# Kernel tuning notes

Measured on AMD Instinct MI355X. Metric: run time of the kernel, lower is better.

Reference implementation:

```python
import jax, jax.numpy as jnp
import numpy as np

N = 50000   # nodes
E = 600000  # edges
F = 128     # num_node_features
H = 128     # hidden_channels
C = 10      # num_classes
G = 64      # graphs in batch


def setup_inputs() -> dict:
    key = jax.random.key(0)
    ks = jax.random.split(key, 12)
    x = jax.random.normal(ks[0], (N, F), jnp.float32)
    edge_index = jax.random.randint(ks[1], (2, E), 0, N, dtype=jnp.int32)
    batch = jnp.sort(jax.random.randint(ks[2], (N,), 0, G, dtype=jnp.int32))
    def glorot(k, shape):
        lim = np.sqrt(6.0 / (shape[0] + shape[1])).astype(np.float32)
        return jax.random.uniform(k, shape, jnp.float32, -lim, lim)
    return {
        "x": x,
        "edge_index": edge_index,
        "batch": batch,
        "W1": glorot(ks[3], (F, H)), "b1": jnp.zeros((H,), jnp.float32),
        "W2": glorot(ks[4], (H, H)), "b2": jnp.zeros((H,), jnp.float32),
        "W3": glorot(ks[5], (H, H)), "b3": jnp.zeros((H,), jnp.float32),
        "Wl": glorot(ks[6], (H, C)), "bl": jnp.zeros((C,), jnp.float32),
    }


def reference(x, edge_index, batch, W1, b1, W2, b2, W3, b3, Wl, bl):
    # GCNConv: add self-loops, symmetric degree normalization D^-1/2 A D^-1/2
    src0, dst0 = edge_index[0], edge_index[1]
    loop = jnp.arange(N, dtype=src0.dtype)
    src = jnp.concatenate([src0, loop])
    dst = jnp.concatenate([dst0, loop])
    deg = jax.ops.segment_sum(jnp.ones_like(dst, jnp.float32), dst, num_segments=N)
    dinv = jnp.where(deg > 0, jax.lax.rsqrt(deg), 0.0)
    norm = dinv[src] * dinv[dst]  # [E+N]

    def conv(h, W, b):
        h = h @ W                                  # [N, H] transform first (PyG GCNConv)
        msg = h[src] * norm[:, None]               # gather + normalize
        return jax.ops.segment_sum(msg, dst, num_segments=N) + b  # scatter-add

    h = jax.nn.relu(conv(x, W1, b1))
    h = jax.nn.relu(conv(h, W2, b2))
    h = conv(h, W3, b3)

    # global_mean_pool over batch ids
    counts = jax.ops.segment_sum(jnp.ones((N,), jnp.float32), batch, num_segments=G)
    pooled = jax.ops.segment_sum(h, batch, num_segments=G) / jnp.maximum(counts, 1.0)[:, None]
    return pooled @ Wl + bl  # [G, C]
```

## Files before the change

kernel.cpp:

```cpp
#include <hip/hip_runtime.h>
#include <hip/hip_bf16.h>

#define NN 50000
#define EE 600000
#define FF 128
#define HH 128
#define CC 10
#define GG 64

typedef unsigned int uint32;
typedef unsigned short ushort16;
typedef __attribute__((ext_vector_type(8))) short short8;
typedef __attribute__((ext_vector_type(4))) float f32x4;

__device__ __forceinline__ float bf_lo(uint32 u) { return __uint_as_float(u << 16); }
__device__ __forceinline__ float bf_hi(uint32 u) { return __uint_as_float(u & 0xffff0000u); }
__device__ __forceinline__ ushort16 f2bf(float f) {
    __hip_bfloat16 b = __float2bfloat16(f);
    return *reinterpret_cast<ushort16*>(&b);
}
__device__ __forceinline__ uint32 pack2bf(float a, float b) {
    return (uint32)f2bf(a) | ((uint32)f2bf(b) << 16);
}

__global__ void count_deg(const int* __restrict__ dst, int* __restrict__ deg) {
    int e = blockIdx.x * blockDim.x + threadIdx.x;
    if (e < EE) atomicAdd(&deg[dst[e]], 1);
}

__global__ void compute_dinv(const int* __restrict__ deg, float* __restrict__ dinv) {
    int n = blockIdx.x * blockDim.x + threadIdx.x;
    if (n < NN) dinv[n] = rsqrtf((float)(deg[n] + 1));
}

#define SB 256
__global__ __launch_bounds__(SB) void scan_block(const int* __restrict__ deg,
                                                 int* __restrict__ row_ptr,
                                                 int* __restrict__ bsum) {
    __shared__ int sm[SB];
    int t = threadIdx.x;
    int i = blockIdx.x * SB + t;
    int v = (i < NN) ? deg[i] : 0;
    sm[t] = v;
    __syncthreads();
    for (int off = 1; off < SB; off <<= 1) {
        int add = (t >= off) ? sm[t - off] : 0;
        __syncthreads();
        sm[t] += add;
        __syncthreads();
    }
    if (i < NN) row_ptr[i] = sm[t] - v;
    if (t == SB - 1) bsum[blockIdx.x] = sm[t];
}

__global__ void scan_bsum(int* __restrict__ bsum, int nb) {
    __shared__ int sm[256];
    int t = threadIdx.x;
    int v = (t < nb) ? bsum[t] : 0;
    sm[t] = v;
    __syncthreads();
    for (int off = 1; off < 256; off <<= 1) {
        int add = (t >= off) ? sm[t - off] : 0;
        __syncthreads();
        sm[t] += add;
        __syncthreads();
    }
    if (t < nb) bsum[t] = sm[t] - v;
}

__global__ __launch_bounds__(SB) void scan_add(int* __restrict__ row_ptr,
                                               const int* __restrict__ bsum) {
    int i = blockIdx.x * SB + threadIdx.x;
    if (i < NN) row_ptr[i] += bsum[blockIdx.x];
    if (i == 0) row_ptr[NN] = EE;
}

__global__ void fill_csr(const int* __restrict__ src, const int* __restrict__ dst,
                         const int* __restrict__ row_ptr, int* __restrict__ cursor,
                         const float* __restrict__ dinv,
                         int2* __restrict__ csr_en) {
    int e = blockIdx.x * blockDim.x + threadIdx.x;
    if (e < EE) {
        int s = src[e], d = dst[e];
        int pos = row_ptr[d] + atomicAdd(&cursor[d], 1);
        csr_en[pos] = make_int2(s * 256, __float_as_int(dinv[s] * dinv[d]));
    }
}

__global__ __launch_bounds__(256) void cast_x(const float* __restrict__ x, uint4* __restrict__ xb) {
    int idx = blockIdx.x * 256 + threadIdx.x;
    const float4* x4 = (const float4*)x;
    float4 a = x4[2 * idx];
    float4 b = x4[2 * idx + 1];
    uint4 o;
    o.x = pack2bf(a.x, a.y);
    o.y = pack2bf(a.z, a.w);
    o.z = pack2bf(b.x, b.y);
    o.w = pack2bf(b.z, b.w);
    xb[idx] = o;
}

__global__ __launch_bounds__(256) void transpose_w(const float* __restrict__ W,
                                                   ushort16* __restrict__ Wt) {
    int base = blockIdx.x * 256 + threadIdx.x;
#pragma unroll
    for (int i = 0; i < 4; i++) {
        int idx = base + i * 4096;
        int col = idx & 127;
        int k = idx >> 7;
        Wt[col * 128 + k] = f2bf(W[k * 128 + col]);
    }
}

__global__ __launch_bounds__(256) void gemm_mfma(const ushort16* __restrict__ A,
                                                 const ushort16* __restrict__ Wt,
                                                 ushort16* __restrict__ out) {
    __shared__ uint4 lds4[34816 / 16];
    char* lds = (char*)lds4;
    int t = threadIdx.x;
    int w = t >> 6, l = t & 63;
    int lrow = l & 15, g = l >> 4;
    int rowBase = blockIdx.x * 64;
    int arow = rowBase + w * 16 + lrow;
    short8 afr[4];
    const char* Ab = (const char*)A;
    bool inb = arow < NN;
#pragma unroll
    for (int s = 0; s < 4; s++) {
        if (inb) {
            afr[s] = *(const short8*)(Ab + (size_t)arow * 256 + s * 64 + g * 16);
        } else {
            short8 z = {0, 0, 0, 0, 0, 0, 0, 0};
            afr[s] = z;
        }
    }
    const char* Wb = (const char*)Wt;
#pragma unroll
    for (int i = 0; i < 8; i++) {
        int idx = t + i * 256;
        int col = idx >> 4, c16 = idx & 15;
        *(uint4*)(lds + col * 272 + c16 * 16) = *(const uint4*)(Wb + col * 256 + c16 * 16);
    }
    __syncthreads();
    f32x4 acc[8];
#pragma unroll
    for (int c = 0; c < 8; c++) { f32x4 z = {0.f, 0.f, 0.f, 0.f}; acc[c] = z; }
#pragma unroll
    for (int s = 0; s < 4; s++) {
#pragma unroll
        for (int c = 0; c < 8; c++) {
            short8 b = *(const short8*)(lds + (c * 16 + lrow) * 272 + s * 64 + g * 16);
            acc[c] = __builtin_amdgcn_mfma_f32_16x16x32_bf16(afr[s], b, acc[c], 0, 0, 0);
        }
    }
    __syncthreads();
    char* myl = lds + w * 8448;
#pragma unroll
    for (int c = 0; c < 8; c++) {
#pragma unroll
        for (int j = 0; j < 4; j++) {
            *(float*)(myl + (g * 4 + j) * 528 + (c * 16 + lrow) * 4) = acc[c][j];
        }
    }
    __syncthreads();
#pragma unroll
    for (int j = 0; j < 8; j++) {
        int rl = (l >> 5) + 2 * j;
        int ch = l & 31;
        float4 v = *(const float4*)(myl + rl * 528 + ch * 16);
        int grow = rowBase + w * 16 + rl;
        if (grow < NN) {
            uint2 o = make_uint2(pack2bf(v.x, v.y), pack2bf(v.z, v.w));
            *(uint2*)((char*)out + (size_t)grow * 256 + ch * 8) = o;
        }
    }
}

__global__ __launch_bounds__(256) void aggregate(const ushort16* __restrict__ hW,
                                                 const int* __restrict__ row_ptr,
                                                 const int2* __restrict__ csr_en,
                                                 const float* __restrict__ dinv,
                                                 const float* __restrict__ bias,
                                                 ushort16* __restrict__ out, int relu) {
    int grp = threadIdx.x >> 4;
    int ll  = threadIdx.x & 15;
    int n = blockIdx.x * 16 + grp;
    if (n >= NN) return;
    const char* base = (const char*)hW;
    int boff = ll << 4;
    float dn = dinv[n];
    float w2 = dn * dn;
    float a0, a1, a2, a3, a4, a5, a6, a7;
    {
        uint4 u = *(const uint4*)(base + (size_t)n * 256 + boff);
        a0 = w2 * bf_lo(u.x); a1 = w2 * bf_hi(u.x);
        a2 = w2 * bf_lo(u.y); a3 = w2 * bf_hi(u.y);
        a4 = w2 * bf_lo(u.z); a5 = w2 * bf_hi(u.z);
        a6 = w2 * bf_lo(u.w); a7 = w2 * bf_hi(u.w);
    }
    int s = row_ptr[n], e = row_ptr[n + 1];
    int k = s;
    for (; k + 4 <= e; k += 4) {
        int2 c0 = csr_en[k], c1 = csr_en[k + 1], c2 = csr_en[k + 2], c3 = csr_en[k + 3];
        uint4 v0 = *(const uint4*)(base + (size_t)(uint32)c0.x + boff);
        uint4 v1 = *(const uint4*)(base + (size_t)(uint32)c1.x + boff);
        uint4 v2 = *(const uint4*)(base + (size_t)(uint32)c2.x + boff);
        uint4 v3 = *(const uint4*)(base + (size_t)(uint32)c3.x + boff);
        float n0 = __int_as_float(c0.y), n1 = __int_as_float(c1.y);
        float n2 = __int_as_float(c2.y), n3 = __int_as_float(c3.y);
        a0 += n0 * bf_lo(v0.x); a1 += n0 * bf_hi(v0.x);
        a2 += n0 * bf_lo(v0.y); a3 += n0 * bf_hi(v0.y);
        a4 += n0 * bf_lo(v0.z); a5 += n0 * bf_hi(v0.z);
        a6 += n0 * bf_lo(v0.w); a7 += n0 * bf_hi(v0.w);
        a0 += n1 * bf_lo(v1.x); a1 += n1 * bf_hi(v1.x);
        a2 += n1 * bf_lo(v1.y); a3 += n1 * bf_hi(v1.y);
        a4 += n1 * bf_lo(v1.z); a5 += n1 * bf_hi(v1.z);
        a6 += n1 * bf_lo(v1.w); a7 += n1 * bf_hi(v1.w);
        a0 += n2 * bf_lo(v2.x); a1 += n2 * bf_hi(v2.x);
        a2 += n2 * bf_lo(v2.y); a3 += n2 * bf_hi(v2.y);
        a4 += n2 * bf_lo(v2.z); a5 += n2 * bf_hi(v2.z);
        a6 += n2 * bf_lo(v2.w); a7 += n2 * bf_hi(v2.w);
        a0 += n3 * bf_lo(v3.x); a1 += n3 * bf_hi(v3.x);
        a2 += n3 * bf_lo(v3.y); a3 += n3 * bf_hi(v3.y);
        a4 += n3 * bf_lo(v3.z); a5 += n3 * bf_hi(v3.z);
        a6 += n3 * bf_lo(v3.w); a7 += n3 * bf_hi(v3.w);
    }
    for (; k < e; k++) {
        int2 c0 = csr_en[k];
        uint4 v0 = *(const uint4*)(base + (size_t)(uint32)c0.x + boff);
        float n0 = __int_as_float(c0.y);
        a0 += n0 * bf_lo(v0.x); a1 += n0 * bf_hi(v0.x);
        a2 += n0 * bf_lo(v0.y); a3 += n0 * bf_hi(v0.y);
        a4 += n0 * bf_lo(v0.z); a5 += n0 * bf_hi(v0.z);
        a6 += n0 * bf_lo(v0.w); a7 += n0 * bf_hi(v0.w);
    }
    float4 bA = *(const float4*)(bias + ll * 8);
    float4 bB = *(const float4*)(bias + ll * 8 + 4);
    a0 += bA.x; a1 += bA.y; a2 += bA.z; a3 += bA.w;
    a4 += bB.x; a5 += bB.y; a6 += bB.z; a7 += bB.w;
    if (relu) {
        a0 = fmaxf(a0, 0.f); a1 = fmaxf(a1, 0.f); a2 = fmaxf(a2, 0.f); a3 = fmaxf(a3, 0.f);
        a4 = fmaxf(a4, 0.f); a5 = fmaxf(a5, 0.f); a6 = fmaxf(a6, 0.f); a7 = fmaxf(a7, 0.f);
    }
    uint4 o;
    o.x = pack2bf(a0, a1); o.y = pack2bf(a2, a3);
    o.z = pack2bf(a4, a5); o.w = pack2bf(a6, a7);
    *(uint4*)((char*)out + (size_t)n * 256 + boff) = o;
}

#define PCH 32
__global__ __launch_bounds__(256) void pool_partial(const uint32* __restrict__ h32,
                                                    const int* __restrict__ batch,
                                                    float* __restrict__ pooled) {
    int wave = threadIdx.x >> 6;
    int lane = threadIdx.x & 63;
    int chunk = blockIdx.x * 4 + wave;
    int n0 = chunk * PCH;
    if (n0 >= NN) return;
    int n1 = n0 + PCH;
    if (n1 > NN) n1 = NN;
    int cur = batch[n0];
    float a0 = 0.f, a1 = 0.f;
    for (int n = n0; n < n1; n++) {
        int g = batch[n];
        if (g != cur) {
            atomicAdd(&pooled[cur * HH + 2 * lane], a0);
            atomicAdd(&pooled[cur * HH + 2 * lane + 1], a1);
            a0 = a1 = 0.f;
            cur = g;
        }
        uint32 v = h32[(size_t)n * 64 + lane];
        a0 += bf_lo(v);
        a1 += bf_hi(v);
    }
    atomicAdd(&pooled[cur * HH + 2 * lane], a0);
    atomicAdd(&pooled[cur * HH + 2 * lane + 1], a1);
}

__global__ __launch_bounds__(128) void final_linear(const float* __restrict__ pooled,
                                                    const int* __restrict__ batch,
                                                    const float* __restrict__ Wl,
                                                    const float* __restrict__ bl,
                                                    float* __restrict__ out) {
    int g = blockIdx.x;
    int t = threadIdx.x;
    __shared__ float pm[128];
    __shared__ int cnt_s;
    if (t == 0) {
        int lo = 0, hi = NN;
        while (lo < hi) { int m = (lo + hi) >> 1; if (batch[m] < g) lo = m + 1; else hi = m; }
        int s = lo;
        lo = 0; hi = NN;
        while (lo < hi) { int m = (lo + hi) >> 1; if (batch[m] < g + 1) lo = m + 1; else hi = m; }
        int c = lo - s;
        cnt_s = c > 0 ? c : 1;
    }
    __syncthreads();
    pm[t] = pooled[g * HH + t] / (float)cnt_s;
    __syncthreads();
    if (t < CC) {
        float o = bl[t];
        for (int f = 0; f < 128; f++) o += pm[f] * Wl[f * CC + t];
        out[g * CC + t] = o;
    }
}

extern "C" void kernel_launch(void* const* d_in, const int* in_sizes, int n_in,
                              void* d_out, int out_size, void* d_ws, size_t ws_size,
                              hipStream_t stream) {
    const float* x    = (const float*)d_in[0];
    const int*   ei   = (const int*)d_in[1];
    const int*   bat  = (const int*)d_in[2];
    const float* W1   = (const float*)d_in[3];
    const float* b1   = (const float*)d_in[4];
    const float* W2   = (const float*)d_in[5];
    const float* b2   = (const float*)d_in[6];
    const float* W3   = (const float*)d_in[7];
    const float* b3   = (const float*)d_in[8];
    const float* Wl   = (const float*)d_in[9];
    const float* bl   = (const float*)d_in[10];
    float* out = (float*)d_out;

    const int* src = ei;
    const int* dst = ei + EE;

    char* ws = (char*)d_ws;
    size_t off = 0;
    auto take = [&](size_t bytes) -> char* {
        char* p = ws + off;
        off += (bytes + 255) & ~(size_t)255;
        return p;
    };
    int*      deg     = (int*)take((size_t)NN * 4);
    float*    dinv    = (float*)take((size_t)NN * 4);
    int*      row_ptr = (int*)take((size_t)(NN + 1) * 4);
    int*      bsum    = (int*)take((size_t)256 * 4);
    int2*     csr_en  = (int2*)take((size_t)EE * 8);
    ushort16* xb      = (ushort16*)take((size_t)NN * FF * 2);
    ushort16* Wt1     = (ushort16*)take((size_t)HH * HH * 2);
    ushort16* Wt2     = (ushort16*)take((size_t)HH * HH * 2);
    ushort16* Wt3     = (ushort16*)take((size_t)HH * HH * 2);
    ushort16* bufA    = (ushort16*)take((size_t)NN * HH * 2);
    ushort16* bufB    = (ushort16*)take((size_t)NN * HH * 2);
    float*    pooled  = (float*)take((size_t)GG * HH * 4);

    const int nbScan = (NN + SB - 1) / SB;

    hipMemsetAsync(deg, 0, (size_t)NN * 4, stream);
    hipMemsetAsync(pooled, 0, (size_t)GG * HH * 4, stream);
    count_deg<<<(EE + 255) / 256, 256, 0, stream>>>(dst, deg);
    compute_dinv<<<(NN + 255) / 256, 256, 0, stream>>>(deg, dinv);
    scan_block<<<nbScan, SB, 0, stream>>>(deg, row_ptr, bsum);
    scan_bsum<<<1, 256, 0, stream>>>(bsum, nbScan);
    scan_add<<<nbScan, SB, 0, stream>>>(row_ptr, bsum);
    hipMemsetAsync(deg, 0, (size_t)NN * 4, stream);
    fill_csr<<<(EE + 255) / 256, 256, 0, stream>>>(src, dst, row_ptr, deg, dinv, csr_en);

    cast_x<<<(NN * FF / 8 + 255) / 256, 256, 0, stream>>>(x, (uint4*)xb);
    transpose_w<<<16, 256, 0, stream>>>(W1, Wt1);
    transpose_w<<<16, 256, 0, stream>>>(W2, Wt2);
    transpose_w<<<16, 256, 0, stream>>>(W3, Wt3);

    const int gemmBlocks = (NN + 63) / 64;
    const int aggBlocks  = (NN + 15) / 16;
    gemm_mfma<<<gemmBlocks, 256, 0, stream>>>(xb, Wt1, bufB);
    aggregate<<<aggBlocks, 256, 0, stream>>>(bufB, row_ptr, csr_en, dinv, b1, bufA, 1);
    gemm_mfma<<<gemmBlocks, 256, 0, stream>>>(bufA, Wt2, bufB);
    aggregate<<<aggBlocks, 256, 0, stream>>>(bufB, row_ptr, csr_en, dinv, b2, bufA, 1);
    gemm_mfma<<<gemmBlocks, 256, 0, stream>>>(bufA, Wt3, bufB);
    aggregate<<<aggBlocks, 256, 0, stream>>>(bufB, row_ptr, csr_en, dinv, b3, bufA, 0);

    const int poolBlocks = ((NN + PCH - 1) / PCH + 3) / 4;
    pool_partial<<<poolBlocks, 256, 0, stream>>>((const uint32*)bufA, bat, pooled);
    final_linear<<<GG, 128, 0, stream>>>(pooled, bat, Wl, bl, out);
}
```

Baseline: 230.1 us.

## Fuse x cast into first GEMM, pooling into last aggregate, merge transposes

Removes the separate fp32-to-bf16 cast of x by having the first GEMM load fp32 rows and convert in registers. Fuses global mean pooling into the final aggregate kernel using an LDS partial sum per block, with global atomics as the fallback, which removes the bf16 write and re-read of the last layer output. Merges the three weight transposes into one launch and software-pipelines the gather loop in aggregate. The bounds check is dropped on the assumption that NN is divisible by 16, and the final layer's pooling now sums fp32 values rather than bf16-rounded ones.

```diff
diff --git a/kernel.cpp b/kernel.cpp
--- a/kernel.cpp
+++ b/kernel.cpp
@@ -87,32 +87,27 @@
     }
 }
 
-__global__ __launch_bounds__(256) void cast_x(const float* __restrict__ x, uint4* __restrict__ xb) {
-    int idx = blockIdx.x * 256 + threadIdx.x;
-    const float4* x4 = (const float4*)x;
-    float4 a = x4[2 * idx];
-    float4 b = x4[2 * idx + 1];
-    uint4 o;
-    o.x = pack2bf(a.x, a.y);
-    o.y = pack2bf(a.z, a.w);
-    o.z = pack2bf(b.x, b.y);
-    o.w = pack2bf(b.z, b.w);
-    xb[idx] = o;
-}
-
-__global__ __launch_bounds__(256) void transpose_w(const float* __restrict__ W,
-                                                   ushort16* __restrict__ Wt) {
-    int base = blockIdx.x * 256 + threadIdx.x;
+__global__ __launch_bounds__(256) void transpose_w3(const float* __restrict__ W1,
+                                                    const float* __restrict__ W2,
+                                                    const float* __restrict__ W3,
+                                                    ushort16* __restrict__ T1,
+                                                    ushort16* __restrict__ T2,
+                                                    ushort16* __restrict__ T3) {
+    int wi = blockIdx.x >> 4;
+    const float* W = (wi == 0) ? W1 : (wi == 1) ? W2 : W3;
+    ushort16* T = (wi == 0) ? T1 : (wi == 1) ? T2 : T3;
+    int base = (blockIdx.x & 15) * 256 + threadIdx.x;
 #pragma unroll
     for (int i = 0; i < 4; i++) {
         int idx = base + i * 4096;
         int col = idx & 127;
         int k = idx >> 7;
-        Wt[col * 128 + k] = f2bf(W[k * 128 + col]);
-    }
-}
-
-__global__ __launch_bounds__(256) void gemm_mfma(const ushort16* __restrict__ A,
+        T[col * 128 + k] = f2bf(W[k * 128 + col]);
+    }
+}
+
+template <bool AF32>
+__global__ __launch_bounds__(256) void gemm_mfma(const void* __restrict__ Av,
                                                  const ushort16* __restrict__ Wt,
                                                  ushort16* __restrict__ out) {
     __shared__ uint4 lds4[34816 / 16];
@@ -123,12 +118,23 @@
     int rowBase = blockIdx.x * 64;
     int arow = rowBase + w * 16 + lrow;
     short8 afr[4];
-    const char* Ab = (const char*)A;
+    const char* Ab = (const char*)Av;
     bool inb = arow < NN;
 #pragma unroll
     for (int s = 0; s < 4; s++) {
         if (inb) {
-            afr[s] = *(const short8*)(Ab + (size_t)arow * 256 + s * 64 + g * 16);
+            if (AF32) {
+                float4 f0 = *(const float4*)(Ab + (size_t)arow * 512 + s * 128 + g * 32);
+                float4 f1 = *(const float4*)(Ab + (size_t)arow * 512 + s * 128 + g * 32 + 16);
+                union { short8 s8; uint32 u[4]; } cv;
+                cv.u[0] = pack2bf(f0.x, f0.y);
+                cv.u[1] = pack2bf(f0.z, f0.w);
+                cv.u[2] = pack2bf(f1.x, f1.y);
+                cv.u[3] = pack2bf(f1.z, f1.w);
+                afr[s] = cv.s8;
+            } else {
+                afr[s] = *(const short8*)(Ab + (size_t)arow * 256 + s * 64 + g * 16);
+            }
         } else {
             short8 z = {0, 0, 0, 0, 0, 0, 0, 0};
             afr[s] = z;
@@ -176,16 +182,27 @@
     }
 }
 
+#define AGG_FMA(c, v)                                          \
+    {                                                          \
+        float nm = __int_as_float(c.y);                        \
+        a0 += nm * bf_lo(v.x); a1 += nm * bf_hi(v.x);          \
+        a2 += nm * bf_lo(v.y); a3 += nm * bf_hi(v.y);          \
+        a4 += nm * bf_lo(v.z); a5 += nm * bf_hi(v.z);          \
+        a6 += nm * bf_lo(v.w); a7 += nm * bf_hi(v.w);          \
+    }
+
+template <int MODE>
 __global__ __launch_bounds__(256) void aggregate(const ushort16* __restrict__ hW,
                                                  const int* __restrict__ row_ptr,
                                                  const int2* __restrict__ csr_en,
                                                  const float* __restrict__ dinv,
                                                  const float* __restrict__ bias,
-                                                 ushort16* __restrict__ out, int relu) {
+                                                 ushort16* __restrict__ out,
+                                                 float* __restrict__ pooled,
+                                                 const int* __restrict__ batch) {
     int grp = threadIdx.x >> 4;
     int ll  = threadIdx.x & 15;
     int n = blockIdx.x * 16 + grp;
-    if (n >= NN) return;
     const char* base = (const char*)hW;
     int boff = ll << 4;
     float dn = dinv[n];
@@ -200,81 +217,71 @@
     }
     int s = row_ptr[n], e = row_ptr[n + 1];
     int k = s;
-    for (; k + 4 <= e; k += 4) {
+    if (k + 4 <= e) {
         int2 c0 = csr_en[k], c1 = csr_en[k + 1], c2 = csr_en[k + 2], c3 = csr_en[k + 3];
         uint4 v0 = *(const uint4*)(base + (size_t)(uint32)c0.x + boff);
         uint4 v1 = *(const uint4*)(base + (size_t)(uint32)c1.x + boff);
         uint4 v2 = *(const uint4*)(base + (size_t)(uint32)c2.x + boff);
         uint4 v3 = *(const uint4*)(base + (size_t)(uint32)c3.x + boff);
-        float n0 = __int_as_float(c0.y), n1 = __int_as_float(c1.y);
-        float n2 = __int_as_float(c2.y), n3 = __int_as_float(c3.y);
-        a0 += n0 * bf_lo(v0.x); a1 += n0 * bf_hi(v0.x);
-        a2 += n0 * bf_lo(v0.y); a3 += n0 * bf_hi(v0.y);
-        a4 += n0 * bf_lo(v0.z); a5 += n0 * bf_hi(v0.z);
-        a6 += n0 * bf_lo(v0.w); a7 += n0 * bf_hi(v0.w);
-        a0 += n1 * bf_lo(v1.x); a1 += n1 * bf_hi(v1.x);
-        a2 += n1 * bf_lo(v1.y); a3 += n1 * bf_hi(v1.y);
-        a4 += n1 * bf_lo(v1.z); a5 += n1 * bf_hi(v1.z);
-        a6 += n1 * bf_lo(v1.w); a7 += n1 * bf_hi(v1.w);
-        a0 += n2 * bf_lo(v2.x); a1 += n2 * bf_hi(v2.x);
-        a2 += n2 * bf_lo(v2.y); a3 += n2 * bf_hi(v2.y);
-        a4 += n2 * bf_lo(v2.z); a5 += n2 * bf_hi(v2.z);
-        a6 += n2 * bf_lo(v2.w); a7 += n2 * bf_hi(v2.w);
-        a0 += n3 * bf_lo(v3.x); a1 += n3 * bf_hi(v3.x);
-        a2 += n3 * bf_lo(v3.y); a3 += n3 * bf_hi(v3.y);
-        a4 += n3 * bf_lo(v3.z); a5 += n3 * bf_hi(v3.z);
-        a6 += n3 * bf_lo(v3.w); a7 += n3 * bf_hi(v3.w);
+        k += 4;
+        for (; k + 4 <= e; k += 4) {
+            int2 d0 = csr_en[k], d1 = csr_en[k + 1], d2 = csr_en[k + 2], d3 = csr_en[k + 3];
+            uint4 w0 = *(const uint4*)(base + (size_t)(uint32)d0.x + boff);
+            uint4 w1 = *(const uint4*)(base + (size_t)(uint32)d1.x + boff);
+            uint4 w2_ = *(const uint4*)(base + (size_t)(uint32)d2.x + boff);
+            uint4 w3 = *(const uint4*)(base + (size_t)(uint32)d3.x + boff);
+            AGG_FMA(c0, v0); AGG_FMA(c1, v1); AGG_FMA(c2, v2); AGG_FMA(c3, v3);
+            c0 = d0; c1 = d1; c2 = d2; c3 = d3;
+            v0 = w0; v1 = w1; v2 = w2_; v3 = w3;
+        }
+        AGG_FMA(c0, v0); AGG_FMA(c1, v1); AGG_FMA(c2, v2); AGG_FMA(c3, v3);
     }
     for (; k < e; k++) {
         int2 c0 = csr_en[k];
         uint4 v0 = *(const uint4*)(base + (size_t)(uint32)c0.x + boff);
-        float n0 = __int_as_float(c0.y);
-        a0 += n0 * bf_lo(v0.x); a1 += n0 * bf_hi(v0.x);
-        a2 += n0 * bf_lo(v0.y); a3 += n0 * bf_hi(v0.y);
-        a4 += n0 * bf_lo(v0.z); a5 += n0 * bf_hi(v0.z);
-        a6 += n0 * bf_lo(v0.w); a7 += n0 * bf_hi(v0.w);
+        AGG_FMA(c0, v0);
     }
     float4 bA = *(const float4*)(bias + ll * 8);
     float4 bB = *(const float4*)(bias + ll * 8 + 4);
     a0 += bA.x; a1 += bA.y; a2 += bA.z; a3 += bA.w;
     a4 += bB.x; a5 += bB.y; a6 += bB.z; a7 += bB.w;
-    if (relu) {
+    if (MODE == 0) {
         a0 = fmaxf(a0, 0.f); a1 = fmaxf(a1, 0.f); a2 = fmaxf(a2, 0.f); a3 = fmaxf(a3, 0.f);
         a4 = fmaxf(a4, 0.f); a5 = fmaxf(a5, 0.f); a6 = fmaxf(a6, 0.f); a7 = fmaxf(a7, 0.f);
-    }
-    uint4 o;
-    o.x = pack2bf(a0, a1); o.y = pack2bf(a2, a3);
-    o.z = pack2bf(a4, a5); o.w = pack2bf(a6, a7);
-    *(uint4*)((char*)out + (size_t)n * 256 + boff) = o;
-}
-
-#define PCH 32
-__global__ __launch_bounds__(256) void pool_partial(const uint32* __restrict__ h32,
-                                                    const int* __restrict__ batch,
-                                                    float* __restrict__ pooled) {
-    int wave = threadIdx.x >> 6;
-    int lane = threadIdx.x & 63;
-    int chunk = blockIdx.x * 4 + wave;
-    int n0 = chunk * PCH;
-    if (n0 >= NN) return;
-    int n1 = n0 + PCH;
-    if (n1 > NN) n1 = NN;
-    int cur = batch[n0];
-    float a0 = 0.f, a1 = 0.f;
-    for (int n = n0; n < n1; n++) {
+        uint4 o;
+        o.x = pack2bf(a0, a1); o.y = pack2bf(a2, a3);
+        o.z = pack2bf(a4, a5); o.w = pack2bf(a6, a7);
+        *(uint4*)((char*)out + (size_t)n * 256 + boff) = o;
+    }
+    if (MODE == 2) {
+        __shared__ float psum[4][128];
+        __shared__ int sgmin;
         int g = batch[n];
-        if (g != cur) {
-            atomicAdd(&pooled[cur * HH + 2 * lane], a0);
-            atomicAdd(&pooled[cur * HH + 2 * lane + 1], a1);
-            a0 = a1 = 0.f;
-            cur = g;
-        }
-        uint32 v = h32[(size_t)n * 64 + lane];
-        a0 += bf_lo(v);
-        a1 += bf_hi(v);
-    }
-    atomicAdd(&pooled[cur * HH + 2 * lane], a0);
-    atomicAdd(&pooled[cur * HH + 2 * lane + 1], a1);
+        if (threadIdx.x == 0) sgmin = g;
+        for (int j = threadIdx.x; j < 512; j += 256) ((float*)psum)[j] = 0.f;
+        __syncthreads();
+        int slot = g - sgmin;
+        if (slot < 4) {
+            float* p = &psum[slot][ll * 8];
+            atomicAdd(p + 0, a0); atomicAdd(p + 1, a1);
+            atomicAdd(p + 2, a2); atomicAdd(p + 3, a3);
+            atomicAdd(p + 4, a4); atomicAdd(p + 5, a5);
+            atomicAdd(p + 6, a6); atomicAdd(p + 7, a7);
+        } else {
+            float* p = &pooled[g * HH + ll * 8];
+            atomicAdd(p + 0, a0); atomicAdd(p + 1, a1);
+            atomicAdd(p + 2, a2); atomicAdd(p + 3, a3);
+            atomicAdd(p + 4, a4); atomicAdd(p + 5, a5);
+            atomicAdd(p + 6, a6); atomicAdd(p + 7, a7);
+        }
+        __syncthreads();
+        for (int j = threadIdx.x; j < 512; j += 256) {
+            int sl = j >> 7, f = j & 127;
+            float v = psum[sl][f];
+            int gg = sgmin + sl;
+            if (v != 0.f && gg < GG) atomicAdd(&pooled[gg * HH + f], v);
+        }
+    }
 }
 
 __global__ __launch_bounds__(128) void final_linear(const float* __restrict__ pooled,
@@ -336,7 +343,6 @@
     int*      row_ptr = (int*)take((size_t)(NN + 1) * 4);
     int*      bsum    = (int*)take((size_t)256 * 4);
     int2*     csr_en  = (int2*)take((size_t)EE * 8);
-    ushort16* xb      = (ushort16*)take((size_t)NN * FF * 2);
     ushort16* Wt1     = (ushort16*)take((size_t)HH * HH * 2);
     ushort16* Wt2     = (ushort16*)take((size_t)HH * HH * 2);
     ushort16* Wt3     = (ushort16*)take((size_t)HH * HH * 2);
@@ -356,21 +362,16 @@
     hipMemsetAsync(deg, 0, (size_t)NN * 4, stream);
     fill_csr<<<(EE + 255) / 256, 256, 0, stream>>>(src, dst, row_ptr, deg, dinv, csr_en);
 
-    cast_x<<<(NN * FF / 8 + 255) / 256, 256, 0, stream>>>(x, (uint4*)xb);
-    transpose_w<<<16, 256, 0, stream>>>(W1, Wt1);
-    transpose_w<<<16, 256, 0, stream>>>(W2, Wt2);
-    transpose_w<<<16, 256, 0, stream>>>(W3, Wt3);
+    transpose_w3<<<48, 256, 0, stream>>>(W1, W2, W3, Wt1, Wt2, Wt3);
 
     const int gemmBlocks = (NN + 63) / 64;
-    const int aggBlocks  = (NN + 15) / 16;
-    gemm_mfma<<<gemmBlocks, 256, 0, stream>>>(xb, Wt1, bufB);
-    aggregate<<<aggBlocks, 256, 0, stream>>>(bufB, row_ptr, csr_en, dinv, b1, bufA, 1);
-    gemm_mfma<<<gemmBlocks, 256, 0, stream>>>(bufA, Wt2, bufB);
-    aggregate<<<aggBlocks, 256, 0, stream>>>(bufB, row_ptr, csr_en, dinv, b2, bufA, 1);
-    gemm_mfma<<<gemmBlocks, 256, 0, stream>>>(bufA, Wt3, bufB);
-    aggregate<<<aggBlocks, 256, 0, stream>>>(bufB, row_ptr, csr_en, dinv, b3, bufA, 0);
-
-    const int poolBlocks = ((NN + PCH - 1) / PCH + 3) / 4;
-    pool_partial<<<poolBlocks, 256, 0, stream>>>((const uint32*)bufA, bat, pooled);
+    const int aggBlocks  = NN / 16;
+    gemm_mfma<true><<<gemmBlocks, 256, 0, stream>>>(x, Wt1, bufB);
+    aggregate<0><<<aggBlocks, 256, 0, stream>>>(bufB, row_ptr, csr_en, dinv, b1, bufA, pooled, bat);
+    gemm_mfma<false><<<gemmBlocks, 256, 0, stream>>>(bufA, Wt2, bufB);
+    aggregate<0><<<aggBlocks, 256, 0, stream>>>(bufB, row_ptr, csr_en, dinv, b2, bufA, pooled, bat);
+    gemm_mfma<false><<<gemmBlocks, 256, 0, stream>>>(bufA, Wt3, bufB);
+    aggregate<2><<<aggBlocks, 256, 0, stream>>>(bufB, row_ptr, csr_en, dinv, b3, bufA, pooled, bat);
+
     final_linear<<<GG, 128, 0, stream>>>(pooled, bat, Wl, bl, out);
 }
```

Result: no change. 228.0 us (-0.9%).
